# Kernel optimization log

Measured on AMD Instinct MI355X. Metric: run time of the kernel, lower is better.

## Reference

```python
import jax, jax.numpy as jnp
import numpy as np
from itertools import combinations_with_replacement

LATENT_DIM = 16
N_PARAMS = 2
N_VARS = LATENT_DIM + N_PARAMS  # 18
POLY_ORDER = 3
BATCH = 131072

# Static exponent index tables: for each degree d, an [n_terms_d, d] array of
# variable indices (combinations with replacement), matching a sympy-style
# polynomial library [1, x_i, x_i*x_j, x_i*x_j*x_k, ...].
IDX = [np.array(list(combinations_with_replacement(range(N_VARS), d)), dtype=np.int32)
       for d in range(1, POLY_ORDER + 1)]
P = 1 + sum(a.shape[0] for a in IDX)  # 1330 library terms


def setup_inputs() -> dict:
    key = jax.random.key(0)
    k1, k2, k3 = jax.random.split(key, 3)
    z = jax.random.normal(k1, (BATCH, LATENT_DIM), dtype=jnp.float32)
    betas = jax.random.normal(k2, (BATCH, N_PARAMS), dtype=jnp.float32)
    big_xi = jax.random.normal(k3, (P, N_VARS), dtype=jnp.float32) * 0.1
    mask = jnp.ones((P, N_VARS), dtype=jnp.float32)
    return {"z": z, "betas": betas, "big_xi": big_xi, "mask": mask}


def _theta(x):
    # x: [B, N_VARS] -> theta: [B, P]
    cols = [jnp.ones((x.shape[0], 1), dtype=x.dtype)]  # constant term
    for idx in IDX:
        acc = x[:, idx[:, 0]]                # [B, n_terms_d]
        for k in range(1, idx.shape[1]):     # loop over degree (<= POLY_ORDER)
            acc = acc * x[:, idx[:, k]]
        cols.append(acc)
    return jnp.concatenate(cols, axis=1)


def reference(z, betas, big_xi, mask):
    x = jnp.concatenate([z, betas], axis=1)  # [B, N_VARS]
    theta = _theta(x)                        # [B, P]
    return theta @ (big_xi * mask)           # [B, N_VARS]
```

## Files before the change

### kernel.cpp

```cpp
#include <hip/hip_runtime.h>
#include <hip/hip_bf16.h>
#include <utility>


constexpr int NVARS   = 18;
constexpr int NOUT    = 18;
constexpr int NROWS   = 131072;
constexpr int PTERMS  = 1330;
constexpr int NCHUNKS = 43;
constexpr int NSLOTS  = NCHUNKS * 8;

typedef __attribute__((ext_vector_type(8))) short short8;
typedef __attribute__((ext_vector_type(4))) float f32x4;

struct T3 { int a, b, c; };

constexpr int rho1(int v) {
    if (v < 16)  return (v & ~3) | ((v + 1) & 3);
    if (v == 16) return 17;
    if (v == 17) return 16;
    return v;
}
constexpr int rho2v(int v) { return rho1(rho1(v)); }

constexpr T3 sort3(int u0, int u1, int u2) {
    int t = 0;
    if (u0 > u1) { t = u0; u0 = u1; u1 = t; }
    if (u1 > u2) { t = u1; u1 = u2; u2 = t; }
    if (u0 > u1) { t = u0; u0 = u1; u1 = t; }
    return T3{u0, u1, u2};
}
constexpr T3 rho3(T3 t) { return sort3(rho1(t.a), rho1(t.b), rho1(t.c)); }

constexpr bool t3_less(T3 x, T3 y) {
    if (x.a != y.a) return x.a < y.a;
    if (x.b != y.b) return x.b < y.b;
    return x.c < y.c;
}
constexpr bool t3_eq(T3 x, T3 y) { return x.a == y.a && x.b == y.b && x.c == y.c; }

constexpr int rank_of(T3 t) {
    int deg = (t.a < 18) + (t.b < 18) + (t.c < 18);
    if (deg == 0) return 0;
    if (deg == 1) return 1 + t.a;
    if (deg == 2) {
        int r = 19;
        for (int a = 0; a < t.a; ++a) r += 18 - a;
        return r + (t.b - t.a);
    }
    int r = 190;
    for (int a = 0; a < t.a; ++a) { int n = 18 - a; r += n * (n + 1) / 2; }
    for (int b = t.a; b < t.b; ++b) r += 18 - b;
    return r + (t.c - t.b);
}

struct RepTables {
    signed char va[NSLOTS], vb[NSLOTS], vc[NSLOTS];
    short p[4][NSLOTS];
    int count;
};

constexpr void consider(RepTables& R, int& s, T3 t) {
    T3 im[4] = {t, T3{0, 0, 0}, T3{0, 0, 0}, T3{0, 0, 0}};
    im[1] = rho3(im[0]);
    im[2] = rho3(im[1]);
    im[3] = rho3(im[2]);
    for (int g = 1; g < 4; ++g)
        if (t3_less(im[g], t)) return;
    R.va[s] = (signed char)t.a; R.vb[s] = (signed char)t.b; R.vc[s] = (signed char)t.c;
    for (int g = 0; g < 4; ++g) {
        bool dup = false;
        for (int h = 0; h < g; ++h)
            if (t3_eq(im[h], im[g])) dup = true;
        R.p[g][s] = dup ? (short)-1 : (short)rank_of(im[g]);
    }
    ++s;
}

constexpr RepTables make_tables() {
    RepTables R{};
    int s = 0;
    consider(R, s, T3{18, 18, 18});
    for (int a = 0; a < NVARS; ++a) consider(R, s, T3{a, 18, 18});
    for (int a = 0; a < NVARS; ++a)
        for (int b = a; b < NVARS; ++b) consider(R, s, T3{a, b, 18});
    for (int a = 0; a < NVARS; ++a)
        for (int b = a; b < NVARS; ++b)
            for (int c = b; c < NVARS; ++c) consider(R, s, T3{a, b, c});
    R.count = s;
    for (; s < NSLOTS; ++s) {
        R.va[s] = 19; R.vb[s] = 19; R.vc[s] = 19;
        for (int g = 0; g < 4; ++g) R.p[g][s] = -1;
    }
    return R;
}

constexpr RepTables h_tab = make_tables();
static_assert(h_tab.count == 342, "orbit enumeration must give 342 rep slots");
__device__ const RepTables d_tab = make_tables();


#if __has_builtin(__builtin_amdgcn_cvt_pk_bf16_f32)
typedef __bf16 bf16x2 __attribute__((ext_vector_type(2)));
__device__ __forceinline__ unsigned pack2(float f0, float f1) {
    bf16x2 r = __builtin_amdgcn_cvt_pk_bf16_f32(f0, f1);
    return __builtin_bit_cast(unsigned, r);
}
#else
__device__ __forceinline__ unsigned pack2(float f0, float f1) {
    unsigned u0 = __float_as_uint(f0) + 0x8000u;
    unsigned u1 = __float_as_uint(f1) + 0x8000u;
    return __builtin_amdgcn_perm(u1, u0, 0x07060302u);
}
#endif


template <int S>
__device__ __forceinline__ float term_val(const float (&x)[NVARS]) {
    constexpr int a = h_tab.va[S], b = h_tab.vb[S], c = h_tab.vc[S];
    if constexpr (a >= 19)      return 0.0f;
    else if constexpr (a == 18) return 1.0f;
    else if constexpr (b == 18) return x[a];
    else if constexpr (c == 18) return x[a] * x[b];
    else                        return x[a] * x[b] * x[c];
}

union AFrag { unsigned u[4]; short8 v; };

template <int CI, int... I>
__device__ __forceinline__ void eval8(const float (&x)[NVARS], float (&t)[8],
                                      std::integer_sequence<int, I...>) {
    ((t[I] = term_val<CI * 8 + I>(x)), ...);
}

template <int CI>
__device__ __forceinline__ void kstep(const float (&x)[NVARS],
                                      const short* __restrict__ wlane,
                                      f32x4& acc0, f32x4& acc1) {
    float t[8];
    eval8<CI>(x, t, std::make_integer_sequence<int, 8>{});
    AFrag af;
#pragma unroll
    for (int j = 0; j < 4; ++j) af.u[j] = pack2(t[2 * j], t[2 * j + 1]);
    short8 b0 = *(const short8*)(wlane + (CI * 2 + 0) * 512);
    short8 b1 = *(const short8*)(wlane + (CI * 2 + 1) * 512);
    acc0 = __builtin_amdgcn_mfma_f32_16x16x32_bf16(af.v, b0, acc0, 0, 0, 0);
    acc1 = __builtin_amdgcn_mfma_f32_16x16x32_bf16(af.v, b1, acc1, 0, 0, 0);
}

template <int... CI>
__device__ __forceinline__ void kloop(const float (&x)[NVARS],
                                      const short* __restrict__ wlane,
                                      f32x4& acc0, f32x4& acc1,
                                      std::integer_sequence<int, CI...>) {
    (kstep<CI>(x, wlane, acc0, acc1), ...);
}

__global__ __launch_bounds__(256, 5) void vindy_mfma(const float* __restrict__ z,
                                                     const float* __restrict__ betas,
                                                     const short* __restrict__ wf,
                                                     float* __restrict__ out) {
    const int lane = threadIdx.x & 63;
    const int wave = threadIdx.x >> 6;
    const int g    = lane >> 4;
    const int mcol = lane & 15;
    const int rowbase = blockIdx.x * 64 + wave * 16;
    const int arow = rowbase + mcol;

    float x0[NVARS];
    {
        const float4* z4 = (const float4*)(z + (size_t)arow * 16);
        float4 v0 = z4[0], v1 = z4[1], v2 = z4[2], v3 = z4[3];
        x0[0]  = v0.x; x0[1]  = v0.y; x0[2]  = v0.z; x0[3]  = v0.w;
        x0[4]  = v1.x; x0[5]  = v1.y; x0[6]  = v1.z; x0[7]  = v1.w;
        x0[8]  = v2.x; x0[9]  = v2.y; x0[10] = v2.z; x0[11] = v2.w;
        x0[12] = v3.x; x0[13] = v3.y; x0[14] = v3.z; x0[15] = v3.w;
        const float2 b2 = *(const float2*)(betas + (size_t)arow * 2);
        x0[16] = b2.x; x0[17] = b2.y;
    }
    const bool s1 = (g & 1) != 0;
    const bool s2 = (g & 2) != 0;
    float y[NVARS], x[NVARS];
#pragma unroll
    for (int v = 0; v < NVARS; ++v) y[v] = s1 ? x0[rho1(v)] : x0[v];
#pragma unroll
    for (int v = 0; v < NVARS; ++v) x[v] = s2 ? y[rho2v(v)] : y[v];

    f32x4 acc0, acc1;
#pragma unroll
    for (int i = 0; i < 4; ++i) { acc0[i] = 0.0f; acc1[i] = 0.0f; }

    const short* wlane = wf + lane * 8;
    kloop(x, wlane, acc0, acc1, std::make_integer_sequence<int, NCHUNKS>{});

    const int orow = rowbase + g * 4;
    float* op0 = out + (size_t)orow * NOUT + mcol;
#pragma unroll
    for (int r = 0; r < 4; ++r) op0[(size_t)r * NOUT] = acc0[r];
    if (mcol < NOUT - 16) {
        float* op1 = out + (size_t)orow * NOUT + 16 + mcol;
#pragma unroll
        for (int r = 0; r < 4; ++r) op1[(size_t)r * NOUT] = acc1[r];
    }
}


__global__ void prep_wfrag(const float* __restrict__ xi, const float* __restrict__ mask,
                           __hip_bfloat16* __restrict__ wf) {
    int i = blockIdx.x * blockDim.x + threadIdx.x;
    if (i >= NCHUNKS * 2 * 64 * 8) return;
    int j  = i & 7;
    int l  = (i >> 3) & 63;
    int ct = i >> 9;
    int c  = ct >> 1;
    int T  = ct & 1;
    int gg = l >> 4;
    int n  = T * 16 + (l & 15);
    int s  = c * 8 + j;
    int p  = (int)d_tab.p[gg][s];
    float v = 0.0f;
    if (p >= 0 && n < NOUT) v = xi[p * NOUT + n] * mask[p * NOUT + n];
    wf[i] = __float2bfloat16(v);
}

extern "C" void kernel_launch(void* const* d_in, const int* in_sizes, int n_in,
                              void* d_out, int out_size, void* d_ws, size_t ws_size,
                              hipStream_t stream) {
    const float* z     = (const float*)d_in[0];
    const float* betas = (const float*)d_in[1];
    const float* xi    = (const float*)d_in[2];
    const float* mask  = (const float*)d_in[3];
    __hip_bfloat16* wf = (__hip_bfloat16*)d_ws;
    float* out = (float*)d_out;

    const int nprep = NCHUNKS * 2 * 64 * 8;
    prep_wfrag<<<(nprep + 255) / 256, 256, 0, stream>>>(xi, mask, wf);
    vindy_mfma<<<NROWS / 64, 256, 0, stream>>>(z, betas, (const short*)d_ws, out);
}
```

Before: 92.82 us.

## Stage weight fragments in LDS, compact output tile, two row tiles per wave

Each wave now processes two 16-row tiles against the same B fragments, so every weight load from memory serves two MFMAs. The whole weight fragment set (a compacted layout in which the second 16-column tile holds only the two real output columns) is copied into shared memory once per block. Per-lane B fragments are then read from LDS rather than global memory or L2. This adds ~49KB of LDS per block, more registers (four accumulators, two x vectors), halves the grid and lowers launch bounds occupancy from 5 to 4.

```diff
diff --git a/kernel.cpp b/kernel.cpp
--- a/kernel.cpp
+++ b/kernel.cpp
@@ -9,6 +9,10 @@
 constexpr int PTERMS  = 1330;
 constexpr int NCHUNKS = 43;
 constexpr int NSLOTS  = NCHUNKS * 8;
+
+constexpr int WF0_SHORTS = NCHUNKS * 512;
+constexpr int WF1_SHORTS = NCHUNKS * 64;
+constexpr int WF_SHORTS  = WF0_SHORTS + WF1_SHORTS;
 
 typedef __attribute__((ext_vector_type(8))) short short8;
 typedef __attribute__((ext_vector_type(4))) float f32x4;
@@ -126,6 +130,7 @@
 }
 
 union AFrag { unsigned u[4]; short8 v; };
+union BFrag { unsigned u[4]; short8 v; };
 
 template <int CI, int... I>
 __device__ __forceinline__ void eval8(const float (&x)[NVARS], float (&t)[8],
@@ -134,73 +139,106 @@
 }
 
 template <int CI>
-__device__ __forceinline__ void kstep(const float (&x)[NVARS],
-                                      const short* __restrict__ wlane,
-                                      f32x4& acc0, f32x4& acc1) {
-    float t[8];
-    eval8<CI>(x, t, std::make_integer_sequence<int, 8>{});
-    AFrag af;
-#pragma unroll
-    for (int j = 0; j < 4; ++j) af.u[j] = pack2(t[2 * j], t[2 * j + 1]);
-    short8 b0 = *(const short8*)(wlane + (CI * 2 + 0) * 512);
-    short8 b1 = *(const short8*)(wlane + (CI * 2 + 1) * 512);
-    acc0 = __builtin_amdgcn_mfma_f32_16x16x32_bf16(af.v, b0, acc0, 0, 0, 0);
-    acc1 = __builtin_amdgcn_mfma_f32_16x16x32_bf16(af.v, b1, acc1, 0, 0, 0);
+__device__ __forceinline__ void kstep(const float (&xA)[NVARS], const float (&xB)[NVARS],
+                                      const short* p0, const short* p1, unsigned zmask,
+                                      f32x4& acc00, f32x4& acc01,
+                                      f32x4& acc10, f32x4& acc11) {
+    float tA[8], tB[8];
+    eval8<CI>(xA, tA, std::make_integer_sequence<int, 8>{});
+    eval8<CI>(xB, tB, std::make_integer_sequence<int, 8>{});
+    AFrag afA, afB;
+#pragma unroll
+    for (int j = 0; j < 4; ++j) {
+        afA.u[j] = pack2(tA[2 * j], tA[2 * j + 1]);
+        afB.u[j] = pack2(tB[2 * j], tB[2 * j + 1]);
+    }
+    short8 b0 = *(const short8*)(p0 + CI * 512);
+    BFrag b1;
+    b1.v = *(const short8*)(p1 + CI * 64);
+#pragma unroll
+    for (int j = 0; j < 4; ++j) b1.u[j] &= zmask;
+    acc00 = __builtin_amdgcn_mfma_f32_16x16x32_bf16(afA.v, b0,   acc00, 0, 0, 0);
+    acc10 = __builtin_amdgcn_mfma_f32_16x16x32_bf16(afB.v, b0,   acc10, 0, 0, 0);
+    acc01 = __builtin_amdgcn_mfma_f32_16x16x32_bf16(afA.v, b1.v, acc01, 0, 0, 0);
+    acc11 = __builtin_amdgcn_mfma_f32_16x16x32_bf16(afB.v, b1.v, acc11, 0, 0, 0);
 }
 
 template <int... CI>
-__device__ __forceinline__ void kloop(const float (&x)[NVARS],
-                                      const short* __restrict__ wlane,
-                                      f32x4& acc0, f32x4& acc1,
+__device__ __forceinline__ void kloop(const float (&xA)[NVARS], const float (&xB)[NVARS],
+                                      const short* p0, const short* p1, unsigned zmask,
+                                      f32x4& acc00, f32x4& acc01,
+                                      f32x4& acc10, f32x4& acc11,
                                       std::integer_sequence<int, CI...>) {
-    (kstep<CI>(x, wlane, acc0, acc1), ...);
-}
-
-__global__ __launch_bounds__(256, 5) void vindy_mfma(const float* __restrict__ z,
+    (kstep<CI>(xA, xB, p0, p1, zmask, acc00, acc01, acc10, acc11), ...);
+}
+
+__device__ __forceinline__ void load_x(const float* __restrict__ z,
+                                       const float* __restrict__ betas,
+                                       int arow, bool s1, bool s2, float (&x)[NVARS]) {
+    float x0[NVARS];
+    const float4* z4 = (const float4*)(z + (size_t)arow * 16);
+    float4 v0 = z4[0], v1 = z4[1], v2 = z4[2], v3 = z4[3];
+    x0[0]  = v0.x; x0[1]  = v0.y; x0[2]  = v0.z; x0[3]  = v0.w;
+    x0[4]  = v1.x; x0[5]  = v1.y; x0[6]  = v1.z; x0[7]  = v1.w;
+    x0[8]  = v2.x; x0[9]  = v2.y; x0[10] = v2.z; x0[11] = v2.w;
+    x0[12] = v3.x; x0[13] = v3.y; x0[14] = v3.z; x0[15] = v3.w;
+    const float2 b2 = *(const float2*)(betas + (size_t)arow * 2);
+    x0[16] = b2.x; x0[17] = b2.y;
+    float y[NVARS];
+#pragma unroll
+    for (int v = 0; v < NVARS; ++v) y[v] = s1 ? x0[rho1(v)] : x0[v];
+#pragma unroll
+    for (int v = 0; v < NVARS; ++v) x[v] = s2 ? y[rho2v(v)] : y[v];
+}
+
+__global__ __launch_bounds__(256, 4) void vindy_mfma(const float* __restrict__ z,
                                                      const float* __restrict__ betas,
                                                      const short* __restrict__ wf,
                                                      float* __restrict__ out) {
+    __shared__ __align__(16) short ldsW[WF_SHORTS];
+    {
+        const float4* src = (const float4*)wf;
+        float4* dst = (float4*)ldsW;
+        for (int i = threadIdx.x; i < WF_SHORTS / 8; i += 256) dst[i] = src[i];
+    }
+    __syncthreads();
+
     const int lane = threadIdx.x & 63;
     const int wave = threadIdx.x >> 6;
     const int g    = lane >> 4;
-    const int mcol = lane & 15;
-    const int rowbase = blockIdx.x * 64 + wave * 16;
-    const int arow = rowbase + mcol;
-
-    float x0[NVARS];
-    {
-        const float4* z4 = (const float4*)(z + (size_t)arow * 16);
-        float4 v0 = z4[0], v1 = z4[1], v2 = z4[2], v3 = z4[3];
-        x0[0]  = v0.x; x0[1]  = v0.y; x0[2]  = v0.z; x0[3]  = v0.w;
-        x0[4]  = v1.x; x0[5]  = v1.y; x0[6]  = v1.z; x0[7]  = v1.w;
-        x0[8]  = v2.x; x0[9]  = v2.y; x0[10] = v2.z; x0[11] = v2.w;
-        x0[12] = v3.x; x0[13] = v3.y; x0[14] = v3.z; x0[15] = v3.w;
-        const float2 b2 = *(const float2*)(betas + (size_t)arow * 2);
-        x0[16] = b2.x; x0[17] = b2.y;
-    }
+    const int n    = lane & 15;
+    const int rowbase = blockIdx.x * 128 + wave * 32;
+
     const bool s1 = (g & 1) != 0;
     const bool s2 = (g & 2) != 0;
-    float y[NVARS], x[NVARS];
-#pragma unroll
-    for (int v = 0; v < NVARS; ++v) y[v] = s1 ? x0[rho1(v)] : x0[v];
-#pragma unroll
-    for (int v = 0; v < NVARS; ++v) x[v] = s2 ? y[rho2v(v)] : y[v];
-
-    f32x4 acc0, acc1;
-#pragma unroll
-    for (int i = 0; i < 4; ++i) { acc0[i] = 0.0f; acc1[i] = 0.0f; }
-
-    const short* wlane = wf + lane * 8;
-    kloop(x, wlane, acc0, acc1, std::make_integer_sequence<int, NCHUNKS>{});
-
-    const int orow = rowbase + g * 4;
-    float* op0 = out + (size_t)orow * NOUT + mcol;
-#pragma unroll
-    for (int r = 0; r < 4; ++r) op0[(size_t)r * NOUT] = acc0[r];
-    if (mcol < NOUT - 16) {
-        float* op1 = out + (size_t)orow * NOUT + 16 + mcol;
-#pragma unroll
-        for (int r = 0; r < 4; ++r) op1[(size_t)r * NOUT] = acc1[r];
+    float xA[NVARS], xB[NVARS];
+    load_x(z, betas, rowbase + n,      s1, s2, xA);
+    load_x(z, betas, rowbase + 16 + n, s1, s2, xB);
+
+    const unsigned zmask = (n < 2) ? 0xFFFFFFFFu : 0u;
+    const short* p0 = ldsW + lane * 8;
+    const short* p1 = ldsW + WF0_SHORTS + (g * 2 + (n < 2 ? n : 0)) * 8;
+
+    f32x4 acc00, acc01, acc10, acc11;
+#pragma unroll
+    for (int i = 0; i < 4; ++i) { acc00[i] = 0.0f; acc01[i] = 0.0f; acc10[i] = 0.0f; acc11[i] = 0.0f; }
+
+    kloop(xA, xB, p0, p1, zmask, acc00, acc01, acc10, acc11,
+          std::make_integer_sequence<int, NCHUNKS>{});
+
+    float* o0 = out + (size_t)(rowbase + g * 4) * NOUT;
+    float* o1 = out + (size_t)(rowbase + 16 + g * 4) * NOUT;
+#pragma unroll
+    for (int r = 0; r < 4; ++r) {
+        o0[(size_t)r * NOUT + n] = acc00[r];
+        o1[(size_t)r * NOUT + n] = acc10[r];
+    }
+    if (n < 2) {
+#pragma unroll
+        for (int r = 0; r < 4; ++r) {
+            o0[(size_t)r * NOUT + 16 + n] = acc01[r];
+            o1[(size_t)r * NOUT + 16 + n] = acc11[r];
+        }
     }
 }
 
@@ -208,18 +246,20 @@
 __global__ void prep_wfrag(const float* __restrict__ xi, const float* __restrict__ mask,
                            __hip_bfloat16* __restrict__ wf) {
     int i = blockIdx.x * blockDim.x + threadIdx.x;
-    if (i >= NCHUNKS * 2 * 64 * 8) return;
-    int j  = i & 7;
-    int l  = (i >> 3) & 63;
-    int ct = i >> 9;
-    int c  = ct >> 1;
-    int T  = ct & 1;
-    int gg = l >> 4;
-    int n  = T * 16 + (l & 15);
-    int s  = c * 8 + j;
-    int p  = (int)d_tab.p[gg][s];
+    if (i >= WF_SHORTS) return;
+    int p = -1, col = 0;
+    if (i < WF0_SHORTS) {
+        int j = i & 7, l = (i >> 3) & 63, c = i >> 9;
+        col = l & 15;
+        p = d_tab.p[l >> 4][c * 8 + j];
+    } else {
+        int i2 = i - WF0_SHORTS;
+        int j = i2 & 7, q = (i2 >> 3) & 7, c = i2 >> 6;
+        col = 16 + (q & 1);
+        p = d_tab.p[q >> 1][c * 8 + j];
+    }
     float v = 0.0f;
-    if (p >= 0 && n < NOUT) v = xi[p * NOUT + n] * mask[p * NOUT + n];
+    if (p >= 0) v = xi[p * NOUT + col] * mask[p * NOUT + col];
     wf[i] = __float2bfloat16(v);
 }
 
@@ -233,7 +273,6 @@
     __hip_bfloat16* wf = (__hip_bfloat16*)d_ws;
     float* out = (float*)d_out;
 
-    const int nprep = NCHUNKS * 2 * 64 * 8;
-    prep_wfrag<<<(nprep + 255) / 256, 256, 0, stream>>>(xi, mask, wf);
-    vindy_mfma<<<NROWS / 64, 256, 0, stream>>>(z, betas, (const short*)d_ws, out);
-}
+    prep_wfrag<<<(WF_SHORTS + 255) / 256, 256, 0, stream>>>(xi, mask, wf);
+    vindy_mfma<<<NROWS / 128, 256, 0, stream>>>(z, betas, (const short*)d_ws, out);
+}
```

Result: faster. 90.45 us (-2.6%).
